# Kernel optimization log

Measured on AMD Instinct MI355X. Metric: run time of the kernel, lower is better.

The kernel has to match this reference:

```python
import jax, jax.numpy as jnp
import numpy as np

B = 256      # batch
C = 512      # num_classes (independent heads)
F = 768      # BERT pooler_output dim (hard-coded in module)
D = 512      # dense_layer_size


def setup_inputs() -> dict:
    key = jax.random.key(0)
    ks = jax.random.split(key, 7)
    s1 = 1.0 / np.sqrt(F)
    s2 = 1.0 / np.sqrt(D)
    return {
        "x":  jax.random.normal(ks[0], (B, F), dtype=jnp.float32),
        "W1": jax.random.normal(ks[1], (C, F, D), dtype=jnp.float32) * s1,
        "b1": jax.random.normal(ks[2], (C, D), dtype=jnp.float32) * s1,
        "W2": jax.random.normal(ks[3], (C, D, D), dtype=jnp.float32) * s2,
        "b2": jax.random.normal(ks[4], (C, D), dtype=jnp.float32) * s2,
        "W3": jax.random.normal(ks[5], (C, D, 2), dtype=jnp.float32) * s2,
        "b3": jax.random.normal(ks[6], (C, 2), dtype=jnp.float32) * s2,
    }


def reference(x, W1, b1, W2, b2, W3, b3):
    # Batched version of the per-class Python loop:
    # each head: Linear(F,D)-ReLU-(Dropout=identity in eval)-Linear(D,D)-ReLU-Linear(D,2)
    h = jax.nn.relu(jnp.einsum('bf,cfd->bcd', x, W1) + b1[None])        # [B, C, D]
    h = jax.nn.relu(jnp.einsum('bcd,cde->bce', h, W2) + b2[None])        # [B, C, D]
    out = jnp.einsum('bcd,cde->bce', h, W3) + b3[None]                   # [B, C, 2]
    return out
```

## Files before the change

kernel.cpp:

```cpp
#include <hip/hip_runtime.h>
#include <stdint.h>

typedef float f32x4 __attribute__((ext_vector_type(4)));
typedef float f32x2 __attribute__((ext_vector_type(2)));
typedef short bf16x8 __attribute__((ext_vector_type(8)));
typedef uint32_t u32x4 __attribute__((ext_vector_type(4)));

__device__ __forceinline__ uint32_t bf16_rne(float f) {
  uint32_t x = __float_as_uint(f);
  return (x + 0x7FFFu + ((x >> 16) & 1u)) >> 16;
}

__device__ __forceinline__ void ldsbar() {
  asm volatile("s_waitcnt lgkmcnt(0)\n\ts_barrier" ::: "memory");
}

__global__ void cast_x_kernel(const float* __restrict__ x,
                              uint32_t* __restrict__ xb, int n2) {
  int i = blockIdx.x * 256 + threadIdx.x;
  if (i >= n2) return;
  f32x2 v = *(const f32x2*)(x + 2 * i);
  xb[i] = bf16_rne(v[0]) | (bf16_rne(v[1]) << 16);
}

__global__ __launch_bounds__(512, 2) void fused_mlp(
    const uint16_t* __restrict__ xb, const float* __restrict__ W1,
    const float* __restrict__ b1, const float* __restrict__ W2,
    const float* __restrict__ b2, const float* __restrict__ W3,
    const float* __restrict__ b3, float* __restrict__ out) {
  constexpr int H1OFF = 28672;
  __shared__ uint8_t smem[159744];

  const int tid = threadIdx.x;
  const int bid = blockIdx.x;
  const int logical = ((bid & 7) << 7) | (bid >> 3);
  const int c = logical >> 1;
  const int mh = logical & 1;

  const float* W1c = W1 + (size_t)c * (768 * 512);
  const float* W2c = W2 + (size_t)c * (512 * 512);

  const int l = tid & 63, w = tid >> 6;
  const int lr = l & 15, lg = l >> 4;

  ((float*)(smem + 16384))[tid] = b1[(size_t)c * 512 + tid];
  ((float*)(smem + 18432))[tid] = b2[(size_t)c * 512 + tid];
  ((float*)(smem + 20480))[tid] = W3[(size_t)c * 1024 + tid];
  ((float*)(smem + 20480))[tid + 512] = W3[(size_t)c * 1024 + 512 + tid];
  if (tid < 2) ((float*)(smem + 24576))[tid] = b3[c * 2 + tid];

  const uint16_t* Ap1 = xb + (size_t)(mh * 128 + w * 16 + lr) * 768 + lg * 8;
  const int h1rd = H1OFF + (w * 16 + lr) * 1024;

  f32x4 acc[4];
#pragma unroll
  for (int j = 0; j < 4; j++) acc[j] = {0.f, 0.f, 0.f, 0.f};

  auto loadB = [&](const float* Wc, int nts, int ts, float* g) {
    const float* p = Wc + (size_t)(ts * 64 + w * 8) * 512 + nts * 64 + l;
#pragma unroll
    for (int r = 0; r < 8; r++) g[r] = p[(size_t)r * 512];
  };
  auto loadA1 = [&](int ts, bf16x8* a2) {
    a2[0] = *(const bf16x8*)(Ap1 + ts * 64);
    a2[1] = *(const bf16x8*)(Ap1 + ts * 64 + 32);
  };
  auto writeB = [&](const float* g, int buf) {
    u32x4 p;
#pragma unroll
    for (int j = 0; j < 4; j++)
      p[j] = bf16_rne(g[2 * j]) | (bf16_rne(g[2 * j + 1]) << 16);
    *(u32x4*)(smem + buf * 8192 + l * 128 + ((w ^ (l & 7)) << 4)) = p;
  };
  auto compB = [&](int buf, int kk) {
    const uint8_t* s = smem + buf * 8192;
    const int kx = ((lg * 16) ^ ((lr & 7) << 4)) ^ (kk << 6);
    bf16x8 b0 = *(const bf16x8*)(s + (0 * 16 + lr) * 128 + kx);
    bf16x8 b1f = *(const bf16x8*)(s + (1 * 16 + lr) * 128 + kx);
    bf16x8 b2f = *(const bf16x8*)(s + (2 * 16 + lr) * 128 + kx);
    bf16x8 b3f = *(const bf16x8*)(s + (3 * 16 + lr) * 128 + kx);
    struct { bf16x8 b[4]; } r = {{b0, b1f, b2f, b3f}};
    return r;
  };
  auto comp1 = [&](int buf, const bf16x8* a2) {
#pragma unroll
    for (int kk = 0; kk < 2; ++kk) {
      auto bb = compB(buf, kk);
#pragma unroll
      for (int nf = 0; nf < 4; nf++)
        acc[nf] = __builtin_amdgcn_mfma_f32_16x16x32_bf16(a2[kk], bb.b[nf],
                                                          acc[nf], 0, 0, 0);
    }
  };
  auto comp2 = [&](int buf, int ts) {
#pragma unroll
    for (int kk = 0; kk < 2; ++kk) {
      bf16x8 av = *(const bf16x8*)(
          smem + h1rd + ((ts * 8 + ((kk * 4 + lg) ^ (lr & 7))) << 4));
      auto bb = compB(buf, kk);
#pragma unroll
      for (int nf = 0; nf < 4; nf++)
        acc[nf] = __builtin_amdgcn_mfma_f32_16x16x32_bf16(av, bb.b[nf],
                                                          acc[nf], 0, 0, 0);
    }
  };

  float g[4][8];
  bf16x8 a[2][2];

  loadB(W1c, 0, 0, g[0]);
  loadB(W1c, 0, 1, g[1]);
  loadA1(0, a[0]);
  loadB(W1c, 0, 2, g[2]);
  loadA1(1, a[1]);
  loadB(W1c, 0, 3, g[3]);
  writeB(g[0], 0);
  ldsbar();

#pragma unroll 1
  for (int so = 0; so < 8; ++so) {
#pragma unroll
    for (int k = 0; k < 12; ++k) {
      comp1(k & 1, a[k & 1]);
      if (k == 11) {
        const int n0 = so * 64;
#pragma unroll
        for (int nf = 0; nf < 4; nf++) {
          float bv = ((const float*)(smem + 16384))[n0 + nf * 16 + lr];
#pragma unroll
          for (int r = 0; r < 4; r++) {
            int row = w * 16 + lg * 4 + r;
            int ch = so * 8 + nf * 2 + (lr >> 3);
            float v = fmaxf(acc[nf][r] + bv, 0.f);
            *(uint16_t*)(smem + H1OFF + row * 1024 +
                         ((ch ^ (row & 7)) << 4) + (lr & 7) * 2) =
                (uint16_t)bf16_rne(v);
          }
          acc[nf] = {0.f, 0.f, 0.f, 0.f};
        }
      }
      const bool last = (so == 7 && k == 11);
      if (!last) writeB(g[(k + 1) & 3], (k + 1) & 1);
      if (!(so == 7 && k >= 10)) loadA1((k + 2) % 12, a[k & 1]);
      if (!(so == 7 && k >= 8)) {
        int k4 = k + 4;
        loadB(W1c, so + (k4 >= 12), k4 >= 12 ? k4 - 12 : k4, g[k & 3]);
      }
      if (!last) ldsbar();
    }
  }

  float s0[4] = {0.f, 0.f, 0.f, 0.f}, s1[4] = {0.f, 0.f, 0.f, 0.f};
  loadB(W2c, 0, 0, g[0]);
  loadB(W2c, 0, 1, g[1]);
  loadB(W2c, 0, 2, g[2]);
  loadB(W2c, 0, 3, g[3]);
  writeB(g[0], 0);
  ldsbar();

#pragma unroll 1
  for (int so = 0; so < 8; ++so) {
#pragma unroll
    for (int k = 0; k < 8; ++k) {
      comp2(k & 1, k);
      if (k == 7) {
        const int n0 = so * 64;
#pragma unroll
        for (int nf = 0; nf < 4; nf++) {
          float bv = ((const float*)(smem + 18432))[n0 + nf * 16 + lr];
          f32x2 w3p = ((const f32x2*)(smem + 20480))[n0 + nf * 16 + lr];
#pragma unroll
          for (int r = 0; r < 4; r++) {
            float v = fmaxf(acc[nf][r] + bv, 0.f);
            s0[r] += v * w3p[0];
            s1[r] += v * w3p[1];
          }
          acc[nf] = {0.f, 0.f, 0.f, 0.f};
        }
      }
      const bool last = (so == 7 && k == 7);
      if (!last) writeB(g[(k + 1) & 3], (k + 1) & 1);
      if (!(so == 7 && k >= 4)) {
        int k4 = k + 4;
        loadB(W2c, so + (k4 >= 8 ? 1 : 0), k4 & 7, g[k & 3]);
      }
      if (!last) ldsbar();
    }
  }

  f32x2 b3v = *(const f32x2*)(smem + 24576);
#pragma unroll
  for (int r = 0; r < 4; r++) {
#pragma unroll
    for (int d = 1; d < 16; d <<= 1) {
      s0[r] += __shfl_xor(s0[r], d);
      s1[r] += __shfl_xor(s1[r], d);
    }
    if (lr == 0) {
      int row = mh * 128 + w * 16 + lg * 4 + r;
      *(f32x2*)(out + ((size_t)row * 512 + c) * 2) =
          f32x2{s0[r] + b3v[0], s1[r] + b3v[1]};
    }
  }
}

extern "C" void kernel_launch(void* const* d_in, const int* in_sizes, int n_in,
                              void* d_out, int out_size, void* d_ws,
                              size_t ws_size, hipStream_t stream) {
  const float* x = (const float*)d_in[0];
  const float* W1 = (const float*)d_in[1];
  const float* b1 = (const float*)d_in[2];
  const float* W2 = (const float*)d_in[3];
  const float* b2 = (const float*)d_in[4];
  const float* W3 = (const float*)d_in[5];
  const float* b3 = (const float*)d_in[6];
  float* out = (float*)d_out;

  uint8_t* ws = (uint8_t*)d_ws;
  if (ws_size < 393216) return;
  uint32_t* xb = (uint32_t*)ws;

  cast_x_kernel<<<dim3(384), dim3(256), 0, stream>>>(x, xb, 98304);
  fused_mlp<<<dim3(1024), dim3(512), 0, stream>>>(
      (const uint16_t*)xb, W1, b1, W2, b2, W3, b3, out);
}
```

Before: 410.9 us.

## Process full batch per block and keep hidden activations in registers

Each block now handles one class head across all 256 batch rows instead of half the batch. W1 and W2 are therefore streamed and converted once per head rather than twice, halving weight traffic. Each wave computes 32 rows with two M fragments and keeps the layer-1 output in registers (h[8][2][2]) via a small per-wave LDS transpose tile. The change also uses the v_cvt_pk_bf16_f32 instruction for packing, shortens the prefetch ring to depth 3, and fully unrolls the outer loops. The costs are much higher register pressure, which risks spills or reduced occupancy, and only 512 blocks to fill the GPU.

```diff
diff --git a/kernel.cpp b/kernel.cpp
--- a/kernel.cpp
+++ b/kernel.cpp
@@ -28,14 +28,11 @@
     const float* __restrict__ b1, const float* __restrict__ W2,
     const float* __restrict__ b2, const float* __restrict__ W3,
     const float* __restrict__ b3, float* __restrict__ out) {
-  constexpr int H1OFF = 28672;
-  __shared__ uint8_t smem[159744];
+  __shared__ uint8_t smem[98304];
 
   const int tid = threadIdx.x;
   const int bid = blockIdx.x;
-  const int logical = ((bid & 7) << 7) | (bid >> 3);
-  const int c = logical >> 1;
-  const int mh = logical & 1;
+  const int c = ((bid & 7) << 6) | (bid >> 3);
 
   const float* W1c = W1 + (size_t)c * (768 * 512);
   const float* W2c = W2 + (size_t)c * (512 * 512);
@@ -49,159 +46,186 @@
   ((float*)(smem + 20480))[tid + 512] = W3[(size_t)c * 1024 + 512 + tid];
   if (tid < 2) ((float*)(smem + 24576))[tid] = b3[c * 2 + tid];
 
-  const uint16_t* Ap1 = xb + (size_t)(mh * 128 + w * 16 + lr) * 768 + lg * 8;
-  const int h1rd = H1OFF + (w * 16 + lr) * 1024;
-
-  f32x4 acc[4];
-#pragma unroll
-  for (int j = 0; j < 4; j++) acc[j] = {0.f, 0.f, 0.f, 0.f};
-
-  auto loadB = [&](const float* Wc, int nts, int ts, float* g) {
-    const float* p = Wc + (size_t)(ts * 64 + w * 8) * 512 + nts * 64 + l;
+  const uint16_t* Ap = xb + (size_t)(w * 32 + lr) * 768 + lg * 8;
+  uint8_t* T = smem + 32768 + w * 8192;
+  const float* b1s = (const float*)(smem + 16384);
+  const float* b2s = (const float*)(smem + 18432);
+  const f32x2* w3s = (const f32x2*)(smem + 20480);
+
+  f32x4 acc[2][4];
+#pragma unroll
+  for (int i = 0; i < 2; i++)
+#pragma unroll
+    for (int j = 0; j < 4; j++) acc[i][j] = {0.f, 0.f, 0.f, 0.f};
+
+  bf16x8 h[8][2][2];
+
+  auto loadB = [&](const float* Wc, int so, int ts, float* g) {
+    const float* p = Wc + (size_t)(ts * 64 + w * 8) * 512 + so * 64 + l;
 #pragma unroll
     for (int r = 0; r < 8; r++) g[r] = p[(size_t)r * 512];
   };
-  auto loadA1 = [&](int ts, bf16x8* a2) {
-    a2[0] = *(const bf16x8*)(Ap1 + ts * 64);
-    a2[1] = *(const bf16x8*)(Ap1 + ts * 64 + 32);
+  auto loadA = [&](int ts, bf16x8* as) {
+#pragma unroll
+    for (int kk = 0; kk < 2; ++kk)
+#pragma unroll
+      for (int mf = 0; mf < 2; mf++)
+        as[kk * 2 + mf] =
+            *(const bf16x8*)(Ap + ts * 64 + kk * 32 + (size_t)mf * 16 * 768);
   };
   auto writeB = [&](const float* g, int buf) {
-    u32x4 p;
-#pragma unroll
-    for (int j = 0; j < 4; j++)
-      p[j] = bf16_rne(g[2 * j]) | (bf16_rne(g[2 * j + 1]) << 16);
+    uint32_t p0, p1, p2, p3;
+    asm("v_cvt_pk_bf16_f32 %0, %1, %2" : "=v"(p0) : "v"(g[0]), "v"(g[1]));
+    asm("v_cvt_pk_bf16_f32 %0, %1, %2" : "=v"(p1) : "v"(g[2]), "v"(g[3]));
+    asm("v_cvt_pk_bf16_f32 %0, %1, %2" : "=v"(p2) : "v"(g[4]), "v"(g[5]));
+    asm("v_cvt_pk_bf16_f32 %0, %1, %2" : "=v"(p3) : "v"(g[6]), "v"(g[7]));
+    u32x4 p = {p0, p1, p2, p3};
     *(u32x4*)(smem + buf * 8192 + l * 128 + ((w ^ (l & 7)) << 4)) = p;
   };
-  auto compB = [&](int buf, int kk) {
-    const uint8_t* s = smem + buf * 8192;
+  auto compB = [&](const uint8_t* s, int kk, bf16x8* b) {
     const int kx = ((lg * 16) ^ ((lr & 7) << 4)) ^ (kk << 6);
-    bf16x8 b0 = *(const bf16x8*)(s + (0 * 16 + lr) * 128 + kx);
-    bf16x8 b1f = *(const bf16x8*)(s + (1 * 16 + lr) * 128 + kx);
-    bf16x8 b2f = *(const bf16x8*)(s + (2 * 16 + lr) * 128 + kx);
-    bf16x8 b3f = *(const bf16x8*)(s + (3 * 16 + lr) * 128 + kx);
-    struct { bf16x8 b[4]; } r = {{b0, b1f, b2f, b3f}};
-    return r;
-  };
-  auto comp1 = [&](int buf, const bf16x8* a2) {
-#pragma unroll
-    for (int kk = 0; kk < 2; ++kk) {
-      auto bb = compB(buf, kk);
-#pragma unroll
-      for (int nf = 0; nf < 4; nf++)
-        acc[nf] = __builtin_amdgcn_mfma_f32_16x16x32_bf16(a2[kk], bb.b[nf],
-                                                          acc[nf], 0, 0, 0);
-    }
-  };
-  auto comp2 = [&](int buf, int ts) {
-#pragma unroll
-    for (int kk = 0; kk < 2; ++kk) {
-      bf16x8 av = *(const bf16x8*)(
-          smem + h1rd + ((ts * 8 + ((kk * 4 + lg) ^ (lr & 7))) << 4));
-      auto bb = compB(buf, kk);
-#pragma unroll
-      for (int nf = 0; nf < 4; nf++)
-        acc[nf] = __builtin_amdgcn_mfma_f32_16x16x32_bf16(av, bb.b[nf],
-                                                          acc[nf], 0, 0, 0);
-    }
-  };
-
-  float g[4][8];
-  bf16x8 a[2][2];
+#pragma unroll
+    for (int nf = 0; nf < 4; nf++)
+      b[nf] = *(const bf16x8*)(s + (nf * 16 + lr) * 128 + kx);
+  };
+
+  float g[3][8];
+  bf16x8 a[2][4];
 
   loadB(W1c, 0, 0, g[0]);
   loadB(W1c, 0, 1, g[1]);
-  loadA1(0, a[0]);
+  loadA(0, a[0]);
   loadB(W1c, 0, 2, g[2]);
-  loadA1(1, a[1]);
-  loadB(W1c, 0, 3, g[3]);
+  loadA(1, a[1]);
   writeB(g[0], 0);
   ldsbar();
 
-#pragma unroll 1
+#pragma unroll
   for (int so = 0; so < 8; ++so) {
 #pragma unroll
     for (int k = 0; k < 12; ++k) {
-      comp1(k & 1, a[k & 1]);
+      const int t = so * 12 + k;
+      {
+        const uint8_t* s = smem + (t & 1) * 8192;
+#pragma unroll
+        for (int kk = 0; kk < 2; ++kk) {
+          bf16x8 b[4];
+          compB(s, kk, b);
+#pragma unroll
+          for (int mf = 0; mf < 2; mf++)
+#pragma unroll
+            for (int nf = 0; nf < 4; nf++)
+              acc[mf][nf] = __builtin_amdgcn_mfma_f32_16x16x32_bf16(
+                  a[t & 1][kk * 2 + mf], b[nf], acc[mf][nf], 0, 0, 0);
+        }
+      }
       if (k == 11) {
-        const int n0 = so * 64;
-#pragma unroll
-        for (int nf = 0; nf < 4; nf++) {
-          float bv = ((const float*)(smem + 16384))[n0 + nf * 16 + lr];
-#pragma unroll
-          for (int r = 0; r < 4; r++) {
-            int row = w * 16 + lg * 4 + r;
-            int ch = so * 8 + nf * 2 + (lr >> 3);
-            float v = fmaxf(acc[nf][r] + bv, 0.f);
-            *(uint16_t*)(smem + H1OFF + row * 1024 +
-                         ((ch ^ (row & 7)) << 4) + (lr & 7) * 2) =
-                (uint16_t)bf16_rne(v);
+#pragma unroll
+        for (int mf = 0; mf < 2; mf++)
+#pragma unroll
+          for (int nf = 0; nf < 4; nf++) {
+            float bv = b1s[so * 64 + nf * 16 + lr];
+#pragma unroll
+            for (int r = 0; r < 4; r++) {
+              int m = mf * 16 + lg * 4 + r;
+              float v = fmaxf(acc[mf][nf][r] + bv, 0.f);
+              *(uint16_t*)(T + m * 128 +
+                           (((nf * 16 + lr) * 2) ^ ((m & 7) << 4))) =
+                  (uint16_t)bf16_rne(v);
+            }
+            acc[mf][nf] = f32x4{0.f, 0.f, 0.f, 0.f};
           }
-          acc[nf] = {0.f, 0.f, 0.f, 0.f};
-        }
-      }
-      const bool last = (so == 7 && k == 11);
-      if (!last) writeB(g[(k + 1) & 3], (k + 1) & 1);
-      if (!(so == 7 && k >= 10)) loadA1((k + 2) % 12, a[k & 1]);
-      if (!(so == 7 && k >= 8)) {
-        int k4 = k + 4;
-        loadB(W1c, so + (k4 >= 12), k4 >= 12 ? k4 - 12 : k4, g[k & 3]);
-      }
+#pragma unroll
+        for (int kk = 0; kk < 2; kk++)
+#pragma unroll
+          for (int mf = 0; mf < 2; mf++) {
+            int m = mf * 16 + lr;
+            h[so][kk][mf] = *(const bf16x8*)(
+                T + m * 128 + ((kk * 64 + lg * 16) ^ ((m & 7) << 4)));
+          }
+      }
+      const bool last = (t == 95);
+      if (!last) writeB(g[(t + 1) % 3], (t + 1) & 1);
+      if (t + 2 < 96) loadA((t + 2) % 12, a[t & 1]);
+      if (t + 3 < 96) loadB(W1c, (t + 3) / 12, (t + 3) % 12, g[t % 3]);
       if (!last) ldsbar();
     }
   }
 
-  float s0[4] = {0.f, 0.f, 0.f, 0.f}, s1[4] = {0.f, 0.f, 0.f, 0.f};
+  float s0[2][4], s1[2][4];
+#pragma unroll
+  for (int mf = 0; mf < 2; mf++)
+#pragma unroll
+    for (int r = 0; r < 4; r++) {
+      s0[mf][r] = 0.f;
+      s1[mf][r] = 0.f;
+    }
+
   loadB(W2c, 0, 0, g[0]);
   loadB(W2c, 0, 1, g[1]);
   loadB(W2c, 0, 2, g[2]);
-  loadB(W2c, 0, 3, g[3]);
   writeB(g[0], 0);
   ldsbar();
 
-#pragma unroll 1
+#pragma unroll
   for (int so = 0; so < 8; ++so) {
 #pragma unroll
     for (int k = 0; k < 8; ++k) {
-      comp2(k & 1, k);
+      const int t = so * 8 + k;
+      {
+        const uint8_t* s = smem + (t & 1) * 8192;
+#pragma unroll
+        for (int kk = 0; kk < 2; ++kk) {
+          bf16x8 b[4];
+          compB(s, kk, b);
+#pragma unroll
+          for (int mf = 0; mf < 2; mf++)
+#pragma unroll
+            for (int nf = 0; nf < 4; nf++)
+              acc[mf][nf] = __builtin_amdgcn_mfma_f32_16x16x32_bf16(
+                  h[k][kk][mf], b[nf], acc[mf][nf], 0, 0, 0);
+        }
+      }
       if (k == 7) {
-        const int n0 = so * 64;
-#pragma unroll
-        for (int nf = 0; nf < 4; nf++) {
-          float bv = ((const float*)(smem + 18432))[n0 + nf * 16 + lr];
-          f32x2 w3p = ((const f32x2*)(smem + 20480))[n0 + nf * 16 + lr];
-#pragma unroll
-          for (int r = 0; r < 4; r++) {
-            float v = fmaxf(acc[nf][r] + bv, 0.f);
-            s0[r] += v * w3p[0];
-            s1[r] += v * w3p[1];
+#pragma unroll
+        for (int mf = 0; mf < 2; mf++)
+#pragma unroll
+          for (int nf = 0; nf < 4; nf++) {
+            float bv = b2s[so * 64 + nf * 16 + lr];
+            f32x2 wp = w3s[so * 64 + nf * 16 + lr];
+#pragma unroll
+            for (int r = 0; r < 4; r++) {
+              float v = fmaxf(acc[mf][nf][r] + bv, 0.f);
+              s0[mf][r] += v * wp[0];
+              s1[mf][r] += v * wp[1];
+            }
+            acc[mf][nf] = f32x4{0.f, 0.f, 0.f, 0.f};
           }
-          acc[nf] = {0.f, 0.f, 0.f, 0.f};
-        }
-      }
-      const bool last = (so == 7 && k == 7);
-      if (!last) writeB(g[(k + 1) & 3], (k + 1) & 1);
-      if (!(so == 7 && k >= 4)) {
-        int k4 = k + 4;
-        loadB(W2c, so + (k4 >= 8 ? 1 : 0), k4 & 7, g[k & 3]);
-      }
+      }
+      const bool last = (t == 63);
+      if (!last) writeB(g[(t + 1) % 3], (t + 1) & 1);
+      if (t + 3 < 64) loadB(W2c, (t + 3) / 8, (t + 3) % 8, g[t % 3]);
       if (!last) ldsbar();
     }
   }
 
   f32x2 b3v = *(const f32x2*)(smem + 24576);
 #pragma unroll
-  for (int r = 0; r < 4; r++) {
-#pragma unroll
-    for (int d = 1; d < 16; d <<= 1) {
-      s0[r] += __shfl_xor(s0[r], d);
-      s1[r] += __shfl_xor(s1[r], d);
-    }
-    if (lr == 0) {
-      int row = mh * 128 + w * 16 + lg * 4 + r;
-      *(f32x2*)(out + ((size_t)row * 512 + c) * 2) =
-          f32x2{s0[r] + b3v[0], s1[r] + b3v[1]};
-    }
-  }
+  for (int mf = 0; mf < 2; mf++)
+#pragma unroll
+    for (int r = 0; r < 4; r++) {
+      float t0 = s0[mf][r], t1 = s1[mf][r];
+#pragma unroll
+      for (int d = 1; d < 16; d <<= 1) {
+        t0 += __shfl_xor(t0, d);
+        t1 += __shfl_xor(t1, d);
+      }
+      if (lr == 0) {
+        int row = w * 32 + mf * 16 + lg * 4 + r;
+        *(f32x2*)(out + ((size_t)row * 512 + c) * 2) =
+            f32x2{t0 + b3v[0], t1 + b3v[1]};
+      }
+    }
 }
 
 extern "C" void kernel_launch(void* const* d_in, const int* in_sizes, int n_in,
@@ -221,6 +245,6 @@
   uint32_t* xb = (uint32_t*)ws;
 
   cast_x_kernel<<<dim3(384), dim3(256), 0, stream>>>(x, xb, 98304);
-  fused_mlp<<<dim3(1024), dim3(512), 0, stream>>>(
+  fused_mlp<<<dim3(512), dim3(512), 0, stream>>>(
       (const uint16_t*)xb, W1, b1, W2, b2, W3, b3, out);
 }
```

Measured after the change: 575.5 us. +40.0%, slower.
